# Optimization experiments

Measured on AMD Instinct MI355X. Metric: run time of the kernel, lower is better.

Reference implementation:

```python
import jax, jax.numpy as jnp
import numpy as np

HID = 4
IN = 150
LAYERS = 4
OUT = 1
SEQ = 512
BATCH = 256


def setup_inputs() -> dict:
    key = jax.random.key(0)
    ks = jax.random.split(key, 12)
    s = 1.0 / np.sqrt(HID)  # PyTorch LSTM init scale
    inp = {
        "x": jax.random.normal(ks[0], (SEQ, BATCH, IN), dtype=jnp.float32),
        "w_ih0": jax.random.uniform(ks[1], (4 * HID, IN), minval=-s, maxval=s, dtype=jnp.float32),
        "w_hh0": jax.random.uniform(ks[2], (4 * HID, HID), minval=-s, maxval=s, dtype=jnp.float32),
        "b_ih0": jax.random.uniform(ks[3], (4 * HID,), minval=-s, maxval=s, dtype=jnp.float32),
        "b_hh0": jax.random.uniform(ks[4], (4 * HID,), minval=-s, maxval=s, dtype=jnp.float32),
        "w_ih_rest": jax.random.uniform(ks[5], (LAYERS - 1, 4 * HID, HID), minval=-s, maxval=s, dtype=jnp.float32),
        "w_hh_rest": jax.random.uniform(ks[6], (LAYERS - 1, 4 * HID, HID), minval=-s, maxval=s, dtype=jnp.float32),
        "b_ih_rest": jax.random.uniform(ks[7], (LAYERS - 1, 4 * HID), minval=-s, maxval=s, dtype=jnp.float32),
        "b_hh_rest": jax.random.uniform(ks[8], (LAYERS - 1, 4 * HID), minval=-s, maxval=s, dtype=jnp.float32),
        "fc_w": jax.random.uniform(ks[9], (OUT, HID), minval=-s, maxval=s, dtype=jnp.float32),
        "fc_b": jax.random.uniform(ks[10], (OUT,), minval=-s, maxval=s, dtype=jnp.float32),
    }
    return inp


def _lstm_layer(x, w_ih, w_hh, b_ih, b_hh):
    # x: (S, B, D_in). PyTorch gate order: i, f, g, o.
    B = x.shape[1]
    xp = jnp.einsum('sbd,gd->sbg', x, w_ih) + (b_ih + b_hh)  # (S, B, 4H)

    def step(carry, xt):
        h, c = carry
        gates = xt + h @ w_hh.T  # (B, 4H)
        i, f, g, o = jnp.split(gates, 4, axis=-1)
        i = jax.nn.sigmoid(i)
        f = jax.nn.sigmoid(f)
        g = jnp.tanh(g)
        o = jax.nn.sigmoid(o)
        c = f * c + i * g
        h = o * jnp.tanh(c)
        return (h, c), h

    h0 = jnp.zeros((B, HID), dtype=x.dtype)
    c0 = jnp.zeros((B, HID), dtype=x.dtype)
    _, hs = jax.lax.scan(step, (h0, c0), xp)
    return hs  # (S, B, H)


def reference(x, w_ih0, w_hh0, b_ih0, b_hh0, w_ih_rest, w_hh_rest, b_ih_rest, b_hh_rest, fc_w, fc_b):
    h = _lstm_layer(x, w_ih0, w_hh0, b_ih0, b_hh0)
    for l in range(LAYERS - 1):
        h = _lstm_layer(h, w_ih_rest[l], w_hh_rest[l], b_ih_rest[l], b_hh_rest[l])
    s, b, hd = h.shape
    out = h.reshape(s * b, hd) @ fc_w.T + fc_b  # (S*B, OUT)
    return out.reshape(s, b, -1)
```

## Files before the change

kernel.cpp:

```cpp
#include <hip/hip_runtime.h>
#include <hip/hip_bf16.h>

#define SEQ 512
#define BATCH 256
#define IN_DIM 150

#if __has_builtin(__builtin_amdgcn_exp2f)
__device__ __forceinline__ float fexp2(float x){ return __builtin_amdgcn_exp2f(x); }
#else
__device__ __forceinline__ float fexp2(float x){ return exp2f(x); }
#endif
#if __has_builtin(__builtin_amdgcn_rcpf)
__device__ __forceinline__ float frcp(float x){ return __builtin_amdgcn_rcpf(x); }
#else
__device__ __forceinline__ float frcp(float x){ return 1.0f/(x); }
#endif

__device__ __forceinline__ float sigm(float x){ return frcp(1.0f + fexp2(-1.44269504088896341f*x)); }
__device__ __forceinline__ float tanhx(float x){ return 1.0f - 2.0f*frcp(1.0f + fexp2(2.88539008177792681f*x)); }

template<int CTRL>
__device__ __forceinline__ float dppmov(float v){
    return __int_as_float(__builtin_amdgcn_mov_dpp(__float_as_int(v), CTRL, 0xF, 0xF, true));
}

__global__ __launch_bounds__(256) void xproj(const float* __restrict__ x,
                                             const float* __restrict__ w,
                                             const float* __restrict__ bih,
                                             const float* __restrict__ bhh,
                                             float* __restrict__ xp)
{
    __shared__ float wl[16*IN_DIM];
    __shared__ float bl[16];
    for (int i=threadIdx.x; i<16*IN_DIM; i+=256) wl[i] = w[i];
    if (threadIdx.x < 16) bl[threadIdx.x] = bih[threadIdx.x] + bhh[threadIdx.x];
    __syncthreads();

    const int r = blockIdx.x*256 + threadIdx.x;
    const float* xr = x + (size_t)r*IN_DIM;
    float acc[16];
#pragma unroll
    for (int g=0; g<16; ++g) acc[g] = bl[g];
#pragma unroll 5
    for (int dq=0; dq<IN_DIM/2; ++dq) {
        const float2 xv = *(const float2*)(xr + dq*2);
#pragma unroll
        for (int g=0; g<16; ++g) {
            const float2 wv = *(const float2*)(&wl[g*IN_DIM + dq*2]);
            acc[g] += xv.x*wv.x + xv.y*wv.y;
        }
    }
    float4* op = (float4*)(xp + (size_t)r*16);
#pragma unroll
    for (int kk=0; kk<4; ++kk)
        op[kk] = make_float4(acc[kk], acc[4+kk], acc[8+kk], acc[12+kk]);
}

__global__ __launch_bounds__(64) void lstm_pipe(
    const float* __restrict__ xp,
    const float* __restrict__ w_hh0,
    const float* __restrict__ w_ih_r,
    const float* __restrict__ w_hh_r,
    const float* __restrict__ b_ih_r,
    const float* __restrict__ b_hh_r,
    const float* __restrict__ fcw,
    const float* __restrict__ fcb,
    float* __restrict__ out)
{
    const int lane = threadIdx.x;
    const int k  = lane & 3;
    const int l  = (lane >> 2) & 3;
    const int bb = lane >> 4;
    const int b  = blockIdx.x*4 + bb;

    const float* whh = (l==0) ? w_hh0 : (w_hh_r + (size_t)(l-1)*64);
    float whp[4][4], wir[4][4], bias[4], fcp[4];
#pragma unroll
    for (int j=0;j<4;++j) {
        const int row = j*4+k;
#pragma unroll
        for (int m=0;m<4;++m) whp[j][m] = whh[row*4 + (k^m)];
        if (l==0) {
            bias[j] = 0.f;
#pragma unroll
            for (int m=0;m<4;++m) wir[j][m] = (m==j) ? 1.f : 0.f;
        } else {
            const float* wih = w_ih_r + (size_t)(l-1)*64;
            bias[j] = b_ih_r[(l-1)*16+row] + b_hh_r[(l-1)*16+row];
#pragma unroll
            for (int m=0;m<4;++m) wir[j][m] = wih[row*4 + (k^m)];
        }
    }
#pragma unroll
    for (int m=0;m<4;++m) fcp[m] = fcw[k^m];
    const float fcbv = fcb[0];

    const float* xbase = xp + (size_t)b*16 + k*4;

    float h=0.f, c=0.f;
    float a0=0.f,a1=0.f,a2=0.f,a3=0.f;
    float s0=0.f,s1=0.f,s2=0.f,s3=0.f;

    auto LDX = [&](int t)->float4 {
        const int tc = t < SEQ-1 ? t : SEQ-1;
        return *(const float4*)(xbase + (size_t)tc*(BATCH*16));
    };

    auto STEP = [&](float4 xv, int tau) {
        const float x0 = (l==0) ? xv.x : s0;
        const float x1 = (l==0) ? xv.y : s1;
        const float x2 = (l==0) ? xv.z : s2;
        const float x3 = (l==0) ? xv.w : s3;
        float g0 = (bias[0] + ((wir[0][0]*x0 + wir[0][1]*x1) + (wir[0][2]*x2 + wir[0][3]*x3)))
                 + ((whp[0][0]*a0 + whp[0][1]*a1) + (whp[0][2]*a2 + whp[0][3]*a3));
        float g1 = (bias[1] + ((wir[1][0]*x0 + wir[1][1]*x1) + (wir[1][2]*x2 + wir[1][3]*x3)))
                 + ((whp[1][0]*a0 + whp[1][1]*a1) + (whp[1][2]*a2 + whp[1][3]*a3));
        float g2 = (bias[2] + ((wir[2][0]*x0 + wir[2][1]*x1) + (wir[2][2]*x2 + wir[2][3]*x3)))
                 + ((whp[2][0]*a0 + whp[2][1]*a1) + (whp[2][2]*a2 + whp[2][3]*a3));
        float g3 = (bias[3] + ((wir[3][0]*x0 + wir[3][1]*x1) + (wir[3][2]*x2 + wir[3][3]*x3)))
                 + ((whp[3][0]*a0 + whp[3][1]*a1) + (whp[3][2]*a2 + whp[3][3]*a3));
        const float ig = sigm(g0);
        const float fg = sigm(g1);
        const float gg = tanhx(g2);
        const float og = sigm(g3);
        c = fg*c + ig*gg;
        h = og * tanhx(c);
        const int t = tau - l;
        if (t < 0) { h = 0.f; c = 0.f; }
        a0 = h;
        a1 = dppmov<0xB1>(h);
        a2 = dppmov<0x4E>(h);
        a3 = dppmov<0x1B>(h);
        s0 = dppmov<0x114>(a0);
        s1 = dppmov<0x114>(a1);
        s2 = dppmov<0x114>(a2);
        s3 = dppmov<0x114>(a3);
        if (l==3 && k==0 && t >= 0 && t < SEQ) {
            out[(size_t)t*BATCH + b] =
                fcbv + ((fcp[0]*a0 + fcp[1]*a1) + (fcp[2]*a2 + fcp[3]*a3));
        }
    };

    float4 A0=LDX(0), A1=LDX(1), A2=LDX(2), A3=LDX(3);
    for (int tau=0; tau<520; tau+=8) {
        float4 B0=LDX(tau+4), B1=LDX(tau+5), B2=LDX(tau+6), B3=LDX(tau+7);
        STEP(A0,tau);   STEP(A1,tau+1); STEP(A2,tau+2); STEP(A3,tau+3);
        A0=LDX(tau+8);  A1=LDX(tau+9);  A2=LDX(tau+10); A3=LDX(tau+11);
        STEP(B0,tau+4); STEP(B1,tau+5); STEP(B2,tau+6); STEP(B3,tau+7);
    }
}

extern "C" void kernel_launch(void* const* d_in, const int* in_sizes, int n_in,
                              void* d_out, int out_size, void* d_ws, size_t ws_size,
                              hipStream_t stream)
{
    const float* x      = (const float*)d_in[0];
    const float* w_ih0  = (const float*)d_in[1];
    const float* w_hh0  = (const float*)d_in[2];
    const float* b_ih0  = (const float*)d_in[3];
    const float* b_hh0  = (const float*)d_in[4];
    const float* w_ih_r = (const float*)d_in[5];
    const float* w_hh_r = (const float*)d_in[6];
    const float* b_ih_r = (const float*)d_in[7];
    const float* b_hh_r = (const float*)d_in[8];
    const float* fc_w   = (const float*)d_in[9];
    const float* fc_b   = (const float*)d_in[10];
    float* out = (float*)d_out;

    float* xp0 = (float*)d_ws;

    xproj<<<SEQ*BATCH/256, 256, 0, stream>>>(x, w_ih0, b_ih0, b_hh0, xp0);
    lstm_pipe<<<BATCH/4, 64, 0, stream>>>(xp0, w_hh0, w_ih_r, w_hh_r,
                                          b_ih_r, b_hh_r, fc_w, fc_b, out);
}
```

Measured before the change: 270.1 us.

## Prescale gates by log2e, merge reciprocals, stage x via LDS DMA, peel loop

The input projection now uses 64-thread blocks that copy each x tile into LDS with global_load_lds, read weights directly from global memory, and accumulate in two FMA chains. Gate pre-activations and the recurrent weights and biases are pre-multiplied by -log2e or 2log2e, so the cell state is carried in a scaled form. The recurrent step merges the sigmoid and tanh reciprocals into fewer rcp calls by multiplying denominators. The time loop is peeled into prologue, body and epilogue so the main body drops the clamping and masking checks. The merged denominators risk overflow to inf for large gate values, which would change the outputs.

New measurement: 283.8 us. +5.1%, slower.

```diff
diff --git a/kernel.cpp b/kernel.cpp
--- a/kernel.cpp
+++ b/kernel.cpp
@@ -16,47 +16,65 @@
 __device__ __forceinline__ float frcp(float x){ return 1.0f/(x); }
 #endif
 
-__device__ __forceinline__ float sigm(float x){ return frcp(1.0f + fexp2(-1.44269504088896341f*x)); }
-__device__ __forceinline__ float tanhx(float x){ return 1.0f - 2.0f*frcp(1.0f + fexp2(2.88539008177792681f*x)); }
+#define NEG_LOG2E -1.44269504088896341f
+#define TWO_LOG2E  2.88539008177792681f
 
 template<int CTRL>
 __device__ __forceinline__ float dppmov(float v){
     return __int_as_float(__builtin_amdgcn_mov_dpp(__float_as_int(v), CTRL, 0xF, 0xF, true));
 }
 
-__global__ __launch_bounds__(256) void xproj(const float* __restrict__ x,
+__global__ __launch_bounds__(64) void xproj3(const float* __restrict__ x,
                                              const float* __restrict__ w,
                                              const float* __restrict__ bih,
                                              const float* __restrict__ bhh,
                                              float* __restrict__ xp)
 {
-    __shared__ float wl[16*IN_DIM];
-    __shared__ float bl[16];
-    for (int i=threadIdx.x; i<16*IN_DIM; i+=256) wl[i] = w[i];
-    if (threadIdx.x < 16) bl[threadIdx.x] = bih[threadIdx.x] + bhh[threadIdx.x];
-    __syncthreads();
-
-    const int r = blockIdx.x*256 + threadIdx.x;
-    const float* xr = x + (size_t)r*IN_DIM;
-    float acc[16];
-#pragma unroll
-    for (int g=0; g<16; ++g) acc[g] = bl[g];
-#pragma unroll 5
+    __shared__ float xs[64*IN_DIM];
+    const int lane = threadIdx.x;
+    const size_t tilebase = (size_t)blockIdx.x * 64 * IN_DIM;
+
+    {
+        auto gsrc = (const __attribute__((address_space(1))) unsigned int*)(x + tilebase);
+        auto ldst = (__attribute__((address_space(3))) unsigned int*)xs;
+#pragma unroll
+        for (int i=0;i<37;++i)
+            __builtin_amdgcn_global_load_lds(gsrc + (size_t)i*256 + lane*4, ldst + i*256, 16, 0, 0);
+#pragma unroll
+        for (int i=0;i<2;++i)
+            __builtin_amdgcn_global_load_lds(gsrc + 9472 + (size_t)i*64 + lane, ldst + 9472 + i*64, 4, 0, 0);
+        asm volatile("s_waitcnt vmcnt(0)" ::: "memory");
+    }
+
+    float2 acc[16];
+#pragma unroll
+    for (int g=0; g<16; ++g) acc[g] = make_float2(0.f, 0.f);
+    const float* xr = xs + lane*IN_DIM;
+#pragma unroll 3
     for (int dq=0; dq<IN_DIM/2; ++dq) {
-        const float2 xv = *(const float2*)(xr + dq*2);
+        const float2 xv = *(const float2*)(xr + 2*dq);
 #pragma unroll
         for (int g=0; g<16; ++g) {
-            const float2 wv = *(const float2*)(&wl[g*IN_DIM + dq*2]);
-            acc[g] += xv.x*wv.x + xv.y*wv.y;
+            const float2 wv = *(const float2*)(w + g*IN_DIM + 2*dq);
+            acc[g].x = __builtin_fmaf(wv.x, xv.x, acc[g].x);
+            acc[g].y = __builtin_fmaf(wv.y, xv.y, acc[g].y);
         }
     }
-    float4* op = (float4*)(xp + (size_t)r*16);
-#pragma unroll
-    for (int kk=0; kk<4; ++kk)
-        op[kk] = make_float4(acc[kk], acc[4+kk], acc[8+kk], acc[12+kk]);
-}
-
-__global__ __launch_bounds__(64) void lstm_pipe(
+    float gate[16];
+#pragma unroll
+    for (int g=0; g<16; ++g)
+        gate[g] = (acc[g].x + acc[g].y) + (bih[g] + bhh[g]);
+
+    float* op = xp + ((size_t)(blockIdx.x*64 + lane))*16;
+#pragma unroll
+    for (int k=0;k<4;++k) {
+        const float4 o = make_float4(gate[k]*NEG_LOG2E, gate[4+k]*NEG_LOG2E,
+                                     gate[8+k]*TWO_LOG2E, gate[12+k]*NEG_LOG2E);
+        *(float4*)(op + k*4) = o;
+    }
+}
+
+__global__ __launch_bounds__(64) void lstm_pipe3(
     const float* __restrict__ xp,
     const float* __restrict__ w_hh0,
     const float* __restrict__ w_ih_r,
@@ -72,23 +90,27 @@
     const int l  = (lane >> 2) & 3;
     const int bb = lane >> 4;
     const int b  = blockIdx.x*4 + bb;
-
-    const float* whh = (l==0) ? w_hh0 : (w_hh_r + (size_t)(l-1)*64);
+    const bool isL0  = (l==0);
+    const bool isOut = (l==3) && (k==0);
+
+    const float* whh = isL0 ? w_hh0 : (w_hh_r + (size_t)(l-1)*64);
     float whp[4][4], wir[4][4], bias[4], fcp[4];
+    const float sfac[4] = {NEG_LOG2E, NEG_LOG2E, TWO_LOG2E, NEG_LOG2E};
 #pragma unroll
     for (int j=0;j<4;++j) {
         const int row = j*4+k;
-#pragma unroll
-        for (int m=0;m<4;++m) whp[j][m] = whh[row*4 + (k^m)];
-        if (l==0) {
+        const float sj = sfac[j];
+#pragma unroll
+        for (int m=0;m<4;++m) whp[j][m] = sj*whh[row*4 + (k^m)];
+        if (isL0) {
             bias[j] = 0.f;
 #pragma unroll
             for (int m=0;m<4;++m) wir[j][m] = (m==j) ? 1.f : 0.f;
         } else {
             const float* wih = w_ih_r + (size_t)(l-1)*64;
-            bias[j] = b_ih_r[(l-1)*16+row] + b_hh_r[(l-1)*16+row];
-#pragma unroll
-            for (int m=0;m<4;++m) wir[j][m] = wih[row*4 + (k^m)];
+            bias[j] = sj*(b_ih_r[(l-1)*16+row] + b_hh_r[(l-1)*16+row]);
+#pragma unroll
+            for (int m=0;m<4;++m) wir[j][m] = sj*wih[row*4 + (k^m)];
         }
     }
 #pragma unroll
@@ -97,36 +119,47 @@
 
     const float* xbase = xp + (size_t)b*16 + k*4;
 
-    float h=0.f, c=0.f;
+    float h=0.f, cp=0.f;
     float a0=0.f,a1=0.f,a2=0.f,a3=0.f;
     float s0=0.f,s1=0.f,s2=0.f,s3=0.f;
 
     auto LDX = [&](int t)->float4 {
+        return *(const float4*)(xbase + (size_t)t*(BATCH*16));
+    };
+    auto LDXC = [&](int t)->float4 {
         const int tc = t < SEQ-1 ? t : SEQ-1;
         return *(const float4*)(xbase + (size_t)tc*(BATCH*16));
     };
 
-    auto STEP = [&](float4 xv, int tau) {
-        const float x0 = (l==0) ? xv.x : s0;
-        const float x1 = (l==0) ? xv.y : s1;
-        const float x2 = (l==0) ? xv.z : s2;
-        const float x3 = (l==0) ? xv.w : s3;
-        float g0 = (bias[0] + ((wir[0][0]*x0 + wir[0][1]*x1) + (wir[0][2]*x2 + wir[0][3]*x3)))
+    auto STEP = [&](float4 xv, int tau, int phase) __attribute__((always_inline)) {
+        const float u0 = isL0 ? xv.x : s0;
+        const float u1 = isL0 ? xv.y : s1;
+        const float u2 = isL0 ? xv.z : s2;
+        const float u3 = isL0 ? xv.w : s3;
+        float g0 = (bias[0] + ((wir[0][0]*u0 + wir[0][1]*u1) + (wir[0][2]*u2 + wir[0][3]*u3)))
                  + ((whp[0][0]*a0 + whp[0][1]*a1) + (whp[0][2]*a2 + whp[0][3]*a3));
-        float g1 = (bias[1] + ((wir[1][0]*x0 + wir[1][1]*x1) + (wir[1][2]*x2 + wir[1][3]*x3)))
+        float g1 = (bias[1] + ((wir[1][0]*u0 + wir[1][1]*u1) + (wir[1][2]*u2 + wir[1][3]*u3)))
                  + ((whp[1][0]*a0 + whp[1][1]*a1) + (whp[1][2]*a2 + whp[1][3]*a3));
-        float g2 = (bias[2] + ((wir[2][0]*x0 + wir[2][1]*x1) + (wir[2][2]*x2 + wir[2][3]*x3)))
+        float g2 = (bias[2] + ((wir[2][0]*u0 + wir[2][1]*u1) + (wir[2][2]*u2 + wir[2][3]*u3)))
                  + ((whp[2][0]*a0 + whp[2][1]*a1) + (whp[2][2]*a2 + whp[2][3]*a3));
-        float g3 = (bias[3] + ((wir[3][0]*x0 + wir[3][1]*x1) + (wir[3][2]*x2 + wir[3][3]*x3)))
+        float g3 = (bias[3] + ((wir[3][0]*u0 + wir[3][1]*u1) + (wir[3][2]*u2 + wir[3][3]*u3)))
                  + ((whp[3][0]*a0 + whp[3][1]*a1) + (whp[3][2]*a2 + whp[3][3]*a3));
-        const float ig = sigm(g0);
-        const float fg = sigm(g1);
-        const float gg = tanhx(g2);
-        const float og = sigm(g3);
-        c = fg*c + ig*gg;
-        h = og * tanhx(c);
+        const float E0 = fexp2(g0);
+        const float Ef = fexp2(g1);
+        const float E2 = fexp2(g2);
+        const float E3 = fexp2(g3);
+        const float f   = frcp(1.0f + Ef);
+        const float d02 = (1.0f + E0) * (1.0f + E2);
+        const float r02 = frcp(d02);
+        const float nig = __builtin_fmaf(TWO_LOG2E, E2, -TWO_LOG2E);
+        const float ig2 = nig * r02;
+        cp = __builtin_fmaf(f, cp, ig2);
+        const float Ec = fexp2(cp);
+        const float dh = (1.0f + E3) * (1.0f + Ec);
+        const float rh = frcp(dh);
+        h = (Ec - 1.0f) * rh;
         const int t = tau - l;
-        if (t < 0) { h = 0.f; c = 0.f; }
+        if (phase==0) { if (t < 0) { h = 0.f; cp = 0.f; } }
         a0 = h;
         a1 = dppmov<0xB1>(h);
         a2 = dppmov<0x4E>(h);
@@ -135,18 +168,34 @@
         s1 = dppmov<0x114>(a1);
         s2 = dppmov<0x114>(a2);
         s3 = dppmov<0x114>(a3);
-        if (l==3 && k==0 && t >= 0 && t < SEQ) {
-            out[(size_t)t*BATCH + b] =
-                fcbv + ((fcp[0]*a0 + fcp[1]*a1) + (fcp[2]*a2 + fcp[3]*a3));
-        }
+        bool doSt = isOut;
+        if (phase==0) doSt = doSt && (t >= 0);
+        if (phase==2) doSt = doSt && (t < SEQ);
+        if (doSt) out[(size_t)t*BATCH + b] =
+            fcbv + ((fcp[0]*a0 + fcp[1]*a1) + (fcp[2]*a2 + fcp[3]*a3));
     };
 
     float4 A0=LDX(0), A1=LDX(1), A2=LDX(2), A3=LDX(3);
-    for (int tau=0; tau<520; tau+=8) {
-        float4 B0=LDX(tau+4), B1=LDX(tau+5), B2=LDX(tau+6), B3=LDX(tau+7);
-        STEP(A0,tau);   STEP(A1,tau+1); STEP(A2,tau+2); STEP(A3,tau+3);
-        A0=LDX(tau+8);  A1=LDX(tau+9);  A2=LDX(tau+10); A3=LDX(tau+11);
-        STEP(B0,tau+4); STEP(B1,tau+5); STEP(B2,tau+6); STEP(B3,tau+7);
+    float4 B0,B1,B2,B3;
+
+    {
+        const int tau=0;
+        B0=LDX(tau+4); B1=LDX(tau+5); B2=LDX(tau+6); B3=LDX(tau+7);
+        STEP(A0,tau,0); STEP(A1,tau+1,0); STEP(A2,tau+2,0); STEP(A3,tau+3,0);
+        A0=LDX(tau+8); A1=LDX(tau+9); A2=LDX(tau+10); A3=LDX(tau+11);
+        STEP(B0,tau+4,0); STEP(B1,tau+5,0); STEP(B2,tau+6,0); STEP(B3,tau+7,0);
+    }
+    for (int tau=8; tau<496; tau+=8) {
+        B0=LDX(tau+4); B1=LDX(tau+5); B2=LDX(tau+6); B3=LDX(tau+7);
+        STEP(A0,tau,1); STEP(A1,tau+1,1); STEP(A2,tau+2,1); STEP(A3,tau+3,1);
+        A0=LDX(tau+8); A1=LDX(tau+9); A2=LDX(tau+10); A3=LDX(tau+11);
+        STEP(B0,tau+4,1); STEP(B1,tau+5,1); STEP(B2,tau+6,1); STEP(B3,tau+7,1);
+    }
+    for (int tau=496; tau<520; tau+=8) {
+        B0=LDXC(tau+4); B1=LDXC(tau+5); B2=LDXC(tau+6); B3=LDXC(tau+7);
+        STEP(A0,tau,2); STEP(A1,tau+1,2); STEP(A2,tau+2,2); STEP(A3,tau+3,2);
+        A0=LDXC(tau+8); A1=LDXC(tau+9); A2=LDXC(tau+10); A3=LDXC(tau+11);
+        STEP(B0,tau+4,2); STEP(B1,tau+5,2); STEP(B2,tau+6,2); STEP(B3,tau+7,2);
     }
 }
 
@@ -169,7 +218,7 @@
 
     float* xp0 = (float*)d_ws;
 
-    xproj<<<SEQ*BATCH/256, 256, 0, stream>>>(x, w_ih0, b_ih0, b_hh0, xp0);
-    lstm_pipe<<<BATCH/4, 64, 0, stream>>>(xp0, w_hh0, w_ih_r, w_hh_r,
-                                          b_ih_r, b_hh_r, fc_w, fc_b, out);
-}
+    xproj3<<<SEQ*BATCH/64, 64, 0, stream>>>(x, w_ih0, b_ih0, b_hh0, xp0);
+    lstm_pipe3<<<BATCH/4, 64, 0, stream>>>(xp0, w_hh0, w_ih_r, w_hh_r,
+                                           b_ih_r, b_hh_r, fc_w, fc_b, out);
+}
```
